# Kernel tuning notes

Measured on AMD Instinct MI355X. Metric: run time of the kernel, lower is better.

## Reference

```python
import jax, jax.numpy as jnp
import numpy as np

K = 32  # knn neighborhood size (hard-coded in get_graph_feature)
EPS_BN = 1e-5


def _bn(x, g, b):
    # batch-norm (training-mode batch stats) over all axes except the last (channel) axis
    axes = tuple(range(x.ndim - 1))
    m = jnp.mean(x, axis=axes, keepdims=True)
    v = jnp.var(x, axis=axes, keepdims=True)
    return (x - m) * jax.lax.rsqrt(v + EPS_BN) * g + b


def _knn_idx(xt, k):
    # xt: [B, N, C] -> indices of k nearest points [B, N, k] (torch topk on -||xi-xj||^2)
    xx = jnp.sum(xt * xt, axis=-1)                       # [B, N]
    inner = jnp.einsum('bnc,bmc->bnm', xt, xt)           # [B, N, N]
    neg_d2 = -(xx[:, :, None] - 2.0 * inner + xx[:, None, :])
    _, idx = jax.lax.top_k(neg_d2, k)
    return idx


def _graph_feature(x, k=K):
    # x: [B, C, N] -> feature [B, N, k, 2C] matching torch cat((neighbors, center))
    xt = jnp.transpose(x, (0, 2, 1))                     # [B, N, C]
    idx = _knn_idx(xt, k)                                # [B, N, k]
    gathered = jax.vmap(lambda a, i: a[i])(xt, idx)      # [B, N, k, C]
    center = jnp.broadcast_to(xt[:, :, None, :], gathered.shape)
    return jnp.concatenate([gathered, center], axis=-1)


def _dgcnn(x, w1, w2, w3, w4, w5, g1, g2, g3, g4, g5, b1, b2, b3, b4, b5):
    # x: [B, 3, N] -> embeddings [B, emb, N]
    feat = _graph_feature(x)                                         # [B, N, K, 6]
    h = jax.nn.relu(_bn(jnp.einsum('bnkc,oc->bnko', feat, w1), g1, b1))
    x1 = jnp.max(h, axis=2)                                          # [B, N, 64]
    h = jax.nn.relu(_bn(jnp.einsum('bnkc,oc->bnko', h, w2), g2, b2))
    x2 = jnp.max(h, axis=2)
    h = jax.nn.relu(_bn(jnp.einsum('bnkc,oc->bnko', h, w3), g3, b3))
    x3 = jnp.max(h, axis=2)
    h = jax.nn.relu(_bn(jnp.einsum('bnkc,oc->bnko', h, w4), g4, b4))
    x4 = jnp.max(h, axis=2)
    cat = jnp.concatenate([x1, x2, x3, x4], axis=-1)                 # [B, N, 512]
    emb = jax.nn.relu(_bn(jnp.einsum('bnc,oc->bno', cat, w5), g5, b5))
    return jnp.transpose(emb, (0, 2, 1))                             # [B, emb, N]


def _pairwise_distance_batch(x, y):
    # x: [B, c, N], y: [B, c, M] -> euclidean distances [B, N, M] (faithful incl. clamp/mask)
    xx = jnp.sum(x * x, axis=1)                          # [B, N]
    yy = jnp.sum(y * y, axis=1)                          # [B, M]
    inner = jnp.einsum('bcn,bcm->bnm', x, y)
    pd = xx[:, :, None] - 2.0 * inner + yy[:, None, :]
    pd_sq = jnp.where(pd > 0.0, pd, 0.0)
    err = (pd_sq <= 0.0).astype(pd.dtype)
    d = jnp.sqrt(pd_sq + err * 1e-16)
    return d * (1.0 - err)


def setup_inputs() -> dict:
    key = jax.random.key(0)
    ks = jax.random.split(key, 20)
    B, N = 4, 2048
    def w(k, o, i):
        return jax.random.normal(k, (o, i), jnp.float32) * (1.0 / np.sqrt(i))
    inp = {
        'src': jax.random.normal(ks[0], (B, 3, N), jnp.float32),
        'tgt': jax.random.normal(ks[1], (B, 3, N), jnp.float32),
        'w1': w(ks[2], 64, 6), 'w2': w(ks[3], 64, 64), 'w3': w(ks[4], 128, 64),
        'w4': w(ks[5], 256, 128), 'w5': w(ks[6], 512, 512),
        'g1': jnp.ones(64), 'g2': jnp.ones(64), 'g3': jnp.ones(128),
        'g4': jnp.ones(256), 'g5': jnp.ones(512),
        'b1': jnp.zeros(64), 'b2': jnp.zeros(64), 'b3': jnp.zeros(128),
        'b4': jnp.zeros(256), 'b5': jnp.zeros(512),
    }
    return inp


def reference(src, tgt, w1, w2, w3, w4, w5, g1, g2, g3, g4, g5, b1, b2, b3, b4, b5):
    params = (w1, w2, w3, w4, w5, g1, g2, g3, g4, g5, b1, b2, b3, b4, b5)
    f_src = _dgcnn(src, *params)                         # [B, emb, N]
    f_tgt = _dgcnn(tgt, *params)                         # [B, emb, N] (siamese)
    d = _pairwise_distance_batch(f_src, f_tgt)           # [B, N, M]
    scores = jax.nn.softmax(-d, axis=-1)                 # soft correspondence
    src_corr = jnp.einsum('bcm,bnm->bcn', tgt, scores)   # tgt @ scores^T, [B, 3, N]
    return src_corr
```

## Files before the change

kernel.cpp:

```cpp
#include <hip/hip_runtime.h>
#include <hip/hip_bf16.h>
#include <math.h>

#define BB 4
#define NN 2048
#define KK 32
#define GG 2
constexpr int BNr = BB * NN;
constexpr int SGr = BB * NN * KK;
constexpr int SR  = GG * SGr;

typedef __hip_bfloat16 bf16;
typedef __attribute__((ext_vector_type(8))) short bf16x8;
typedef __attribute__((ext_vector_type(4))) float f32x4;
__device__ __forceinline__ float b2f(bf16 v) { return __bfloat162float(v); }
__device__ __forceinline__ bf16  f2b(float v) { return __float2bfloat16(v); }
__device__ __forceinline__ short f2bs(float v) { bf16 b = f2b(v); return *(short*)&b; }
__device__ __forceinline__ float bs2f(short s) { bf16 b; *(short*)&b = s; return b2f(b); }

#define SWZ128(b) ((b) ^ ((((b) >> 7) & 7) << 4))
#define SWZ256(b) ((b) ^ ((((b) >> 8) & 7) << 4))

__global__ __launch_bounds__(256) void knn_kernel(const float* __restrict__ src,
                                                  const float* __restrict__ tgt,
                                                  int* __restrict__ idx_out) {
    __shared__ float pts[3 * NN];
    __shared__ float xxs[NN];
    int blk = blockIdx.x;
    int gb = blk >> 9;
    int chunk = blk & 511;
    int g = gb >> 2, b = gb & 3;
    const float* x = (g == 0 ? src : tgt) + (size_t)b * 3 * NN;
    int t = threadIdx.x;
    for (int i = t; i < 3 * NN; i += 256) pts[i] = x[i];
    __syncthreads();
    for (int m = t; m < NN; m += 256) {
        float p0 = pts[m], p1 = pts[NN + m], p2 = pts[2 * NN + m];
        xxs[m] = p0 * p0 + p1 * p1 + p2 * p2;
    }
    __syncthreads();
    int w = t >> 6, l = t & 63;
    int n = chunk * 4 + w;
    float q0 = pts[n], q1 = pts[NN + n], q2 = pts[2 * NN + n];
    float xxn = xxs[n];
    float d2[32];
#pragma unroll
    for (int s = 0; s < 32; ++s) {
        int m = s * 64 + l;
        float dot = q0 * pts[m] + q1 * pts[NN + m] + q2 * pts[2 * NN + m];
        d2[s] = (xxn - 2.0f * dot) + xxs[m];
    }
    float gval[4]; int gslot[4];
#pragma unroll
    for (int G = 0; G < 4; ++G) {
        float v = d2[G * 8]; int sl = G * 8;
#pragma unroll
        for (int s = 1; s < 8; ++s)
            if (d2[G * 8 + s] < v) { v = d2[G * 8 + s]; sl = G * 8 + s; }
        gval[G] = v; gslot[G] = sl;
    }
    int* outp = idx_out + ((size_t)gb * NN + n) * KK;
    for (int k = 0; k < KK; ++k) {
        float bv = fminf(fminf(gval[0], gval[1]), fminf(gval[2], gval[3]));
        float gv = bv;
#pragma unroll
        for (int off = 1; off < 64; off <<= 1) gv = fminf(gv, __shfl_xor(gv, off));
        unsigned long long mask = __ballot(bv == gv);
        int winner = (int)__builtin_ctzll(mask);
        if (l == winner) {
            int grp = (gval[0] == gv) ? 0 : (gval[1] == gv) ? 1 : (gval[2] == gv) ? 2 : 3;
#pragma unroll
            for (int G = 0; G < 4; ++G)
                if (G == grp) {
                    int bs = gslot[G];
                    outp[k] = bs * 64 + l;
#pragma unroll
                    for (int s = 0; s < 8; ++s)
                        if (G * 8 + s == bs) d2[G * 8 + s] = INFINITY;
                    float v = d2[G * 8]; int sl = G * 8;
#pragma unroll
                    for (int s = 1; s < 8; ++s)
                        if (d2[G * 8 + s] < v) { v = d2[G * 8 + s]; sl = G * 8 + s; }
                    gval[G] = v; gslot[G] = sl;
                }
        }
    }
}

__global__ void zero_kernel(float* __restrict__ p, int n) {
    int i = blockIdx.x * 256 + threadIdx.x;
    if (i < n) p[i] = 0.f;
}

__global__ void cvt_all_kernel(const float* __restrict__ w2, const float* __restrict__ w3,
                               const float* __restrict__ w4, const float* __restrict__ w5,
                               bf16* __restrict__ w2b, bf16* __restrict__ w3b,
                               bf16* __restrict__ w4b, bf16* __restrict__ w5b) {
    int i = blockIdx.x * 256 + threadIdx.x;
    if (i < 4096)   w2b[i] = f2b(w2[i]);
    if (i < 8192)   w3b[i] = f2b(w3[i]);
    if (i < 32768)  w4b[i] = f2b(w4[i]);
    if (i < 262144) w5b[i] = f2b(w5[i]);
}

__global__ void finalize_bn_kernel(float* __restrict__ sums, int C,
                                   const float* __restrict__ gamma,
                                   const float* __restrict__ beta,
                                   float cnt, float* __restrict__ params) {
    int i = blockIdx.x * blockDim.x + threadIdx.x;
    if (i >= GG * C) return;
    int g = i / C, c = i - g * C;
    float s  = sums[(g * 512 + c) * 2 + 0];
    float sq = sums[(g * 512 + c) * 2 + 1];
    float mean = s / cnt;
    float var = sq / cnt - mean * mean;
    if (var < 0.f) var = 0.f;
    float sc = gamma[c] * rsqrtf(var + 1e-5f);
    params[(g * 512 + c) * 2 + 0] = sc;
    params[(g * 512 + c) * 2 + 1] = beta[c] - mean * sc;
    sums[(g * 512 + c) * 2 + 0] = 0.f;
    sums[(g * 512 + c) * 2 + 1] = 0.f;
}

template <int MODE>
__global__ __launch_bounds__(256, 3) void l12_mfma(
    const float* __restrict__ src, const float* __restrict__ tgt,
    const float* __restrict__ w1, const bf16* __restrict__ w2b,
    const int* __restrict__ idx, const float* __restrict__ p1,
    bf16* __restrict__ H2, bf16* __restrict__ cat, float* __restrict__ sums) {
    __shared__ char F1s[32768];
    __shared__ char W2s[8192];
    __shared__ float epiA[512];
    __shared__ float epiB[128];
    int tid = threadIdx.x;
    int w = tid >> 6, l = tid & 63, lg = l >> 4, lr = l & 15;
    long long row0 = (long long)blockIdx.x * 256;
    int g = (int)(row0 / SGr);

    epiA[tid] = 0.f; epiA[tid + 256] = 0.f;
    if (MODE == 1) {
        if (tid < 128) epiB[tid] = 0.f;
        for (int s = tid; s < 512; s += 256)
            *(bf16x8*)(W2s + SWZ128(s * 16)) = *(const bf16x8*)(w2b + s * 8);
    }

    bf16x8 af[4];
#pragma unroll
    for (int i = 0; i < 4; ++i) {
        af[i] = (bf16x8){0, 0, 0, 0, 0, 0, 0, 0};
        if (lg == 0) {
            int rr = (int)row0 + w * 64 + 16 * i + lr;
            int nrow = rr >> 5;
            int n = nrow & (NN - 1);
            int gb = nrow >> 11;
            int b = gb & 3, gg = gb >> 2;
            const float* x = (gg ? tgt : src) + (size_t)b * 3 * NN;
            int j = idx[rr];
            af[i][0] = f2bs(x[j]);
            af[i][1] = f2bs(x[NN + j]);
            af[i][2] = f2bs(x[2 * NN + j]);
            af[i][3] = f2bs(x[n]);
            af[i][4] = f2bs(x[NN + n]);
            af[i][5] = f2bs(x[2 * NN + n]);
        }
    }
    bf16x8 bf1[4];
#pragma unroll
    for (int j = 0; j < 4; ++j) {
        bf1[j] = (bf16x8){0, 0, 0, 0, 0, 0, 0, 0};
        if (lg == 0) {
            int o = 16 * j + lr;
#pragma unroll
            for (int c = 0; c < 6; ++c) bf1[j][c] = f2bs(w1[o * 6 + c]);
        }
    }

    f32x4 acc1[4][4] = {};
#pragma unroll
    for (int i = 0; i < 4; ++i)
#pragma unroll
        for (int j = 0; j < 4; ++j)
            acc1[i][j] = __builtin_amdgcn_mfma_f32_16x16x32_bf16(af[i], bf1[j], acc1[i][j], 0, 0, 0);

    __syncthreads();

    if (MODE == 0) {
#pragma unroll
        for (int j = 0; j < 4; ++j) {
            int c = 16 * j + lr;
            float s = 0.f, q = 0.f;
#pragma unroll
            for (int i = 0; i < 4; ++i)
#pragma unroll
                for (int r = 0; r < 4; ++r) { float v = acc1[i][j][r]; s += v; q += v * v; }
            s += __shfl_xor(s, 16); s += __shfl_xor(s, 32);
            q += __shfl_xor(q, 16); q += __shfl_xor(q, 32);
            if (lg == 0) {
                atomicAdd(&epiA[c * 2], s);
                atomicAdd(&epiA[c * 2 + 1], q);
            }
        }
        __syncthreads();
        if (tid < 128) atomicAdd(&sums[g * 1024 + tid], epiA[tid]);
        return;
    }

#pragma unroll
    for (int j = 0; j < 4; ++j) {
        int c = 16 * j + lr;
        float sc = p1[(g * 512 + c) * 2], sh = p1[(g * 512 + c) * 2 + 1];
#pragma unroll
        for (int i = 0; i < 4; ++i) {
            float m = 0.f;
#pragma unroll
            for (int r = 0; r < 4; ++r) {
                float v = fmaf(acc1[i][j][r], sc, sh);
                v = v > 0.f ? v : 0.f;
                m = fmaxf(m, v);
                int rowi = w * 64 + 16 * i + 4 * lg + r;
                *(bf16*)(F1s + SWZ128((rowi * 64 + c) * 2)) = f2b(v);
            }
            int p = 2 * w + (i >> 1);
            atomicMax((int*)epiA + p * 64 + c, __float_as_int(m));
        }
    }
    __syncthreads();

    {
        long long pt0 = row0 >> 5;
        for (int e = tid; e < 512; e += 256) {
            int p = e >> 6, c = e & 63;
            cat[(pt0 + p) * 512 + c] = f2b(__int_as_float(((int*)epiA)[p * 64 + c]));
        }
    }

    f32x4 acc2[4][4] = {};
#pragma unroll
    for (int ks = 0; ks < 2; ++ks) {
        bf16x8 bv[4];
#pragma unroll
        for (int j = 0; j < 4; ++j)
            bv[j] = *(bf16x8*)(W2s + SWZ128(((16 * j + lr) * 64 + ks * 32 + lg * 8) * 2));
#pragma unroll
        for (int i = 0; i < 4; ++i) {
            bf16x8 a = *(bf16x8*)(F1s + SWZ128(((w * 64 + 16 * i + lr) * 64 + ks * 32 + lg * 8) * 2));
#pragma unroll
            for (int j = 0; j < 4; ++j)
                acc2[i][j] = __builtin_amdgcn_mfma_f32_16x16x32_bf16(a, bv[j], acc2[i][j], 0, 0, 0);
        }
    }

#pragma unroll
    for (int j = 0; j < 4; ++j) {
        int c = 16 * j + lr;
        float s = 0.f, q = 0.f;
#pragma unroll
        for (int i = 0; i < 4; ++i)
#pragma unroll
            for (int r = 0; r < 4; ++r) {
                float v = acc2[i][j][r];
                s += v; q += v * v;
                long long gr = row0 + w * 64 + 16 * i + 4 * lg + r;
                H2[gr * 64 + c] = f2b(v);
            }
        s += __shfl_xor(s, 16); s += __shfl_xor(s, 32);
        q += __shfl_xor(q, 16); q += __shfl_xor(q, 32);
        if (lg == 0) {
            atomicAdd(&epiB[c * 2], s);
            atomicAdd(&epiB[c * 2 + 1], q);
        }
    }
    __syncthreads();
    if (tid < 128) atomicAdd(&sums[g * 1024 + tid], epiB[tid]);
}

template <int APPLY>
__global__ __launch_bounds__(512, 2) void chain34_mfma(
    const bf16* __restrict__ H2, const bf16* __restrict__ w3b,
    const bf16* __restrict__ w4b, const float* __restrict__ p2,
    const float* __restrict__ p3, const float* __restrict__ p4,
    bf16* __restrict__ cat, float* __restrict__ sums) {
    extern __shared__ char smem[];
    char* W3s = smem;
    char* W4s = smem + 16384;
    char* A2s = smem + 81920;
    char* F3s = smem + 98304;
    float* P3s = (float*)(smem + 131072);
    float* P4s = (float*)(smem + 132096);
    float* epi = (float*)(smem + 134144);
    float* P2s = (float*)(smem + 138240);

    int tid = threadIdx.x;
    int w = tid >> 6, l = tid & 63, lg = l >> 4, lr = l & 15;
    long long rowB0 = (long long)blockIdx.x * 512;
    int g = (int)(rowB0 / SGr);

    for (int s = tid; s < 1024; s += 512)
        *(bf16x8*)(W3s + SWZ128(s * 16)) = *(const bf16x8*)(w3b + s * 8);
    for (int s = tid; s < 4096; s += 512)
        *(bf16x8*)(W4s + SWZ256(s * 16)) = *(const bf16x8*)(w4b + s * 8);
    if (tid < 256) P3s[tid] = p3[g * 1024 + tid];
    if (tid < 128) P2s[tid] = p2[g * 1024 + tid];
    P4s[tid] = p4 ? p4[g * 1024 + tid] : 0.f;
    if (!APPLY) epi[tid] = 0.f;
    __syncthreads();

    for (int chunk = 0; chunk < 4; ++chunk) {
        long long row0 = rowB0 + chunk * 128;
        for (int s = tid; s < 1024; s += 512) {
            bf16x8 rv = *(const bf16x8*)(H2 + row0 * 64 + s * 8);
            int cb = (s & 7) * 8;
            bf16x8 ov;
#pragma unroll
            for (int e = 0; e < 8; ++e) {
                float v = fmaf(bs2f(rv[e]), P2s[(cb + e) * 2], P2s[(cb + e) * 2 + 1]);
                v = v > 0.f ? v : 0.f;
                ov[e] = f2bs(v);
            }
            *(bf16x8*)(A2s + SWZ128(s * 16)) = ov;
        }
        if (APPLY) { ((int*)epi)[tid] = 0; ((int*)epi)[tid + 512] = 0; }
        __syncthreads();

        f32x4 acc3[8] = {};
#pragma unroll
        for (int ks = 0; ks < 2; ++ks) {
            bf16x8 a = *(bf16x8*)(A2s + SWZ128(((16 * w + lr) * 64 + ks * 32 + lg * 8) * 2));
#pragma unroll
            for (int j = 0; j < 8; ++j) {
                bf16x8 b = *(bf16x8*)(W3s + SWZ128(((16 * j + lr) * 64 + ks * 32 + lg * 8) * 2));
                acc3[j] = __builtin_amdgcn_mfma_f32_16x16x32_bf16(a, b, acc3[j], 0, 0, 0);
            }
        }
#pragma unroll
        for (int j = 0; j < 8; ++j) {
            int c = 16 * j + lr;
            float sc = P3s[c * 2], sh = P3s[c * 2 + 1];
#pragma unroll
            for (int r = 0; r < 4; ++r) {
                float v = fmaf(acc3[j][r], sc, sh);
                v = v > 0.f ? v : 0.f;
                int rowi = 16 * w + 4 * lg + r;
                *(bf16*)(F3s + SWZ256((rowi * 128 + c) * 2)) = f2b(v);
            }
        }
        __syncthreads();

        f32x4 acc4[16] = {};
#pragma unroll
        for (int ks = 0; ks < 4; ++ks) {
            bf16x8 a = *(bf16x8*)(F3s + SWZ256(((16 * w + lr) * 128 + ks * 32 + lg * 8) * 2));
#pragma unroll
            for (int j = 0; j < 16; ++j) {
                bf16x8 b = *(bf16x8*)(W4s + SWZ256(((16 * j + lr) * 128 + ks * 32 + lg * 8) * 2));
                acc4[j] = __builtin_amdgcn_mfma_f32_16x16x32_bf16(a, b, acc4[j], 0, 0, 0);
            }
        }

        if (!APPLY) {
#pragma unroll
            for (int j = 0; j < 16; ++j) {
                int c = 16 * j + lr;
                float s = acc4[j][0] + acc4[j][1] + acc4[j][2] + acc4[j][3];
                float q = acc4[j][0] * acc4[j][0] + acc4[j][1] * acc4[j][1] +
                          acc4[j][2] * acc4[j][2] + acc4[j][3] * acc4[j][3];
                s += __shfl_xor(s, 16); s += __shfl_xor(s, 32);
                q += __shfl_xor(q, 16); q += __shfl_xor(q, 32);
                if (lg == 0) {
                    atomicAdd(&epi[c * 2], s);
                    atomicAdd(&epi[c * 2 + 1], q);
                }
            }
        } else {
#pragma unroll
            for (int j = 0; j < 16; ++j) {
                int c = 16 * j + lr;
                float sc = P4s[c * 2], sh = P4s[c * 2 + 1];
                float m = 0.f;
#pragma unroll
                for (int r = 0; r < 4; ++r) {
                    float v = fmaf(acc4[j][r], sc, sh);
                    v = v > 0.f ? v : 0.f;
                    m = fmaxf(m, v);
                }
                m = fmaxf(m, __shfl_xor(m, 16));
                m = fmaxf(m, __shfl_xor(m, 32));
                if (lg == 0)
                    atomicMax((int*)epi + (w >> 1) * 256 + c, __float_as_int(m));
            }
            __syncthreads();
            long long pt0 = row0 >> 5;
            for (int e = tid; e < 1024; e += 512) {
                int p = e >> 8, c = e & 255;
                cat[(pt0 + p) * 512 + 256 + c] = f2b(__int_as_float(((int*)epi)[p * 256 + c]));
            }
            {
                int p = tid >> 7, c = tid & 127;
                float m = 0.f;
                for (int r = 0; r < 32; ++r)
                    m = fmaxf(m, b2f(*(bf16*)(F3s + SWZ256(((p * 32 + r) * 128 + c) * 2))));
                cat[(pt0 + p) * 512 + 128 + c] = f2b(m);
            }
            __syncthreads();
        }
    }
    if (!APPLY) {
        __syncthreads();
        atomicAdd(&sums[g * 1024 + tid], epi[tid]);
    }
}

template <int MODE, int CH, int BNA>
__global__ __launch_bounds__(256, 4) void mfma_gemm(
    const bf16* __restrict__ A, const bf16* __restrict__ Wt,
    float* __restrict__ OutF, bf16* __restrict__ OutB,
    int Cin, int ldOut, long long sA, long long sW, long long sO,
    int rowsPerGroup, const float* __restrict__ params, float* __restrict__ sums,
    const float* __restrict__ pba, bf16* __restrict__ cat) {
    __shared__ char As[16384];
    __shared__ char Bs[8192];
    __shared__ float epi[128];
    __shared__ float PBs[128];
    __shared__ int x2m[256];
    int tid = threadIdx.x;
    int w = tid >> 6, l = tid & 63, lg = l >> 4, lr = l & 15;
    int bz = blockIdx.z;
    const bf16* Ap = A + (long long)bz * sA;
    const bf16* Wp = Wt + (long long)bz * sW;
    int o0 = blockIdx.y * 64;
    long long rowB0 = (long long)blockIdx.x * (128 * CH);
    int g = (int)(rowB0 / rowsPerGroup);
    if ((MODE == 1 || MODE == 3) && tid < 128) epi[tid] = 0.f;
    if (BNA && tid < 128) PBs[tid] = pba[g * 1024 + tid];
    int wr = (w >> 1) * 64, wc = (w & 1) * 32;

    for (int ch = 0; ch < CH; ++ch) {
        long long row0 = rowB0 + (long long)ch * 128;
        if (BNA) {
            __syncthreads();
            if (tid < 256) x2m[tid] = 0;
        }
        f32x4 acc[4][2] = {};
        for (int k0 = 0; k0 < Cin; k0 += 64) {
            __syncthreads();
            for (int s = tid; s < 1024; s += 256) {
                if (BNA) {
                    bf16x8 rv = *(const bf16x8*)(Ap + (row0 + (s >> 3)) * Cin + k0 + (s & 7) * 8);
                    int cb = k0 + (s & 7) * 8;
                    int pt = (s >> 3) >> 5;
                    bf16x8 ov;
#pragma unroll
                    for (int e = 0; e < 8; ++e) {
                        float v = fmaf(bs2f(rv[e]), PBs[(cb + e) * 2], PBs[(cb + e) * 2 + 1]);
                        v = v > 0.f ? v : 0.f;
                        ov[e] = f2bs(v);
                        atomicMax(&x2m[pt * 64 + cb + e], __float_as_int(v));
                    }
                    *(bf16x8*)(As + SWZ128(s * 16)) = ov;
                } else {
                    *(bf16x8*)(As + SWZ128(s * 16)) =
                        *(const bf16x8*)(Ap + (row0 + (s >> 3)) * Cin + k0 + (s & 7) * 8);
                }
            }
            for (int s = tid; s < 512; s += 256)
                *(bf16x8*)(Bs + SWZ128(s * 16)) =
                    *(const bf16x8*)(Wp + (long long)(o0 + (s >> 3)) * Cin + k0 + (s & 7) * 8);
            __syncthreads();
#pragma unroll
            for (int ks = 0; ks < 2; ++ks) {
                bf16x8 b0 = *(bf16x8*)(Bs + SWZ128(((wc + lr) * 64 + ks * 32 + lg * 8) * 2));
                bf16x8 b1 = *(bf16x8*)(Bs + SWZ128(((wc + 16 + lr) * 64 + ks * 32 + lg * 8) * 2));
#pragma unroll
                for (int i = 0; i < 4; ++i) {
                    bf16x8 a = *(bf16x8*)(As + SWZ128(((wr + 16 * i + lr) * 64 + ks * 32 + lg * 8) * 2));
                    acc[i][0] = __builtin_amdgcn_mfma_f32_16x16x32_bf16(a, b0, acc[i][0], 0, 0, 0);
                    acc[i][1] = __builtin_amdgcn_mfma_f32_16x16x32_bf16(a, b1, acc[i][1], 0, 0, 0);
                }
            }
        }
        if (BNA && blockIdx.y == 0) {
            long long pt0 = row0 >> 5;
            if (tid < 256) {
                int p = tid >> 6, c = tid & 63;
                cat[(pt0 + p) * 512 + 64 + c] = f2b(__int_as_float(x2m[tid]));
            }
        }
        if (MODE == 1 || MODE == 3) {
#pragma unroll
            for (int j = 0; j < 2; ++j) {
                int c = wc + 16 * j + lr;
                float s = 0.f, q = 0.f;
#pragma unroll
                for (int i = 0; i < 4; ++i)
#pragma unroll
                    for (int r = 0; r < 4; ++r) {
                        float v = acc[i][j][r];
                        s += v; q += v * v;
                    }
                s += __shfl_xor(s, 16); s += __shfl_xor(s, 32);
                q += __shfl_xor(q, 16); q += __shfl_xor(q, 32);
                if (lg == 0) {
                    atomicAdd(&epi[c * 2], s);
                    atomicAdd(&epi[c * 2 + 1], q);
                }
            }
        }
        if (MODE == 0 || MODE == 3) {
            float* Op = OutF + (long long)bz * sO;
#pragma unroll
            for (int j = 0; j < 2; ++j) {
                int gc = o0 + wc + 16 * j + lr;
#pragma unroll
                for (int i = 0; i < 4; ++i)
#pragma unroll
                    for (int r = 0; r < 4; ++r) {
                        long long gr = row0 + wr + 16 * i + 4 * lg + r;
                        Op[gr * ldOut + gc] = acc[i][j][r];
                    }
            }
        }
    }
    if (MODE == 1 || MODE == 3) {
        __syncthreads();
        if (tid < 128) atomicAdd(&sums[g * 1024 + o0 * 2 + tid], epi[tid]);
    }
}

__global__ __launch_bounds__(256) void emb_finalize(const float* __restrict__ h5,
                                                    const float* __restrict__ p5,
                                                    bf16* __restrict__ embB,
                                                    float* __restrict__ nrm) {
    __shared__ float red[256];
    int row = blockIdx.x; int t = threadIdx.x;
    int g = row / BNr;
    float s = 0.f;
#pragma unroll
    for (int i = 0; i < 2; ++i) {
        int c = t + i * 256;
        float v = fmaf(h5[(size_t)row * 512 + c], p5[(g * 512 + c) * 2], p5[(g * 512 + c) * 2 + 1]);
        v = v > 0.f ? v : 0.f;
        bf16 bb = f2b(v);
        embB[(size_t)row * 512 + c] = bb;
        float vb = b2f(bb);
        s += vb * vb;
    }
    red[t] = s; __syncthreads();
    for (int st = 128; st > 0; st >>= 1) { if (t < st) red[t] += red[t + st]; __syncthreads(); }
    if (t == 0) nrm[row] = red[0];
}

__global__ __launch_bounds__(256) void corr_kernel(const float* __restrict__ inner,
                                                   const float* __restrict__ nrm,
                                                   const float* __restrict__ tgt,
                                                   float* __restrict__ out) {
    __shared__ float red[256];
    int blk = blockIdx.x;
    int b = blk >> 11, n = blk & (NN - 1);
    int t = threadIdx.x;
    const float* inr = inner + ((size_t)b * NN + n) * NN;
    float xx = nrm[b * NN + n];
    float dloc[8];
    float vmax = -INFINITY;
#pragma unroll
    for (int i = 0; i < 8; ++i) {
        int m = t + i * 256;
        float pd = (xx - 2.f * inr[m]) + nrm[BNr + b * NN + m];
        float d = pd > 0.f ? sqrtf(pd) : 0.f;
        dloc[i] = d;
        vmax = fmaxf(vmax, -d);
    }
    red[t] = vmax; __syncthreads();
    for (int s = 128; s > 0; s >>= 1) { if (t < s) red[t] = fmaxf(red[t], red[t + s]); __syncthreads(); }
    vmax = red[0]; __syncthreads();
    const float* tp = tgt + (size_t)b * 3 * NN;
    float se = 0.f, s0 = 0.f, s1 = 0.f, s2 = 0.f;
#pragma unroll
    for (int i = 0; i < 8; ++i) {
        int m = t + i * 256;
        float p = expf(-dloc[i] - vmax);
        se += p;
        s0 += p * tp[m]; s1 += p * tp[NN + m]; s2 += p * tp[2 * NN + m];
    }
    red[t] = se; __syncthreads();
    for (int s = 128; s > 0; s >>= 1) { if (t < s) red[t] += red[t + s]; __syncthreads(); }
    float tot = red[0]; __syncthreads();
    red[t] = s0; __syncthreads();
    for (int s = 128; s > 0; s >>= 1) { if (t < s) red[t] += red[t + s]; __syncthreads(); }
    float o0v = red[0]; __syncthreads();
    red[t] = s1; __syncthreads();
    for (int s = 128; s > 0; s >>= 1) { if (t < s) red[t] += red[t + s]; __syncthreads(); }
    float o1v = red[0]; __syncthreads();
    red[t] = s2; __syncthreads();
    for (int s = 128; s > 0; s >>= 1) { if (t < s) red[t] += red[t + s]; __syncthreads(); }
    float o2v = red[0];
    if (t == 0) {
        out[(size_t)b * 3 * NN + n]          = o0v / tot;
        out[(size_t)b * 3 * NN + NN + n]     = o1v / tot;
        out[(size_t)b * 3 * NN + 2 * NN + n] = o2v / tot;
    }
}

extern "C" void kernel_launch(void* const* d_in, const int* in_sizes, int n_in,
                              void* d_out, int out_size, void* d_ws, size_t ws_size,
                              hipStream_t stream) {
    const float* src = (const float*)d_in[0];
    const float* tgt = (const float*)d_in[1];
    const float* w1  = (const float*)d_in[2];
    const float* w2  = (const float*)d_in[3];
    const float* w3  = (const float*)d_in[4];
    const float* w4  = (const float*)d_in[5];
    const float* w5  = (const float*)d_in[6];
    const float* g1  = (const float*)d_in[7];
    const float* g2  = (const float*)d_in[8];
    const float* g3  = (const float*)d_in[9];
    const float* g4  = (const float*)d_in[10];
    const float* g5  = (const float*)d_in[11];
    const float* b1  = (const float*)d_in[12];
    const float* b2  = (const float*)d_in[13];
    const float* b3  = (const float*)d_in[14];
    const float* b4  = (const float*)d_in[15];
    const float* b5  = (const float*)d_in[16];
    float* out = (float*)d_out;
    char* ws = (char*)d_ws;
    (void)in_sizes; (void)n_in;

    size_t off = 0;
    auto alloc = [&](size_t bytes) { size_t o = off; off = (off + bytes + 255) & ~(size_t)255; return o; };
    int*   idx  = (int*)(ws + alloc((size_t)SR * 4));
    bf16*  H2   = (bf16*)(ws + alloc((size_t)SR * 64 * 2));
    bf16*  cat  = (bf16*)(ws + alloc((size_t)GG * BNr * 512 * 2));
    bf16*  embB = (bf16*)(ws + alloc((size_t)GG * BNr * 512 * 2));
    float* h5   = (float*)(ws + alloc((size_t)GG * BNr * 512 * 4));
    float* nrm  = (float*)(ws + alloc((size_t)GG * BNr * 4));
    float* sums = (float*)(ws + alloc(2048 * 4));
    float* prm  = (float*)(ws + alloc(5 * 2048 * 4));
    bf16*  w2b  = (bf16*)(ws + alloc(4096 * 2));
    bf16*  w3b  = (bf16*)(ws + alloc(8192 * 2));
    bf16*  w4b  = (bf16*)(ws + alloc(32768 * 2));
    bf16*  w5b  = (bf16*)(ws + alloc(262144 * 2));
    float* P1 = prm, *P2 = prm + 2048, *P3 = prm + 4096, *P4 = prm + 6144, *P5 = prm + 8192;
    float* inner = (float*)H2;

    if (ws_size < off) {
        hipMemsetAsync(d_out, 0, (size_t)out_size * 4, stream);
        return;
    }

    knn_kernel<<<GG * BB * NN / 4, 256, 0, stream>>>(src, tgt, idx);
    cvt_all_kernel<<<1024, 256, 0, stream>>>(w2, w3, w4, w5, w2b, w3b, w4b, w5b);
    zero_kernel<<<8, 256, 0, stream>>>(sums, 2048);

    l12_mfma<0><<<SR / 256, 256, 0, stream>>>(src, tgt, w1, w2b, idx, nullptr, nullptr, nullptr, sums);
    finalize_bn_kernel<<<1, 128, 0, stream>>>(sums, 64, g1, b1, (float)SGr, P1);

    l12_mfma<1><<<SR / 256, 256, 0, stream>>>(src, tgt, w1, w2b, idx, P1, H2, cat, sums);
    finalize_bn_kernel<<<1, 128, 0, stream>>>(sums, 64, g2, b2, (float)SGr, P2);

    mfma_gemm<1, 4, 1><<<dim3(SR / 512, 2, 1), 256, 0, stream>>>(
        H2, w3b, nullptr, nullptr, 64, 0, 0, 0, 0, SGr, nullptr, sums, P2, cat);
    finalize_bn_kernel<<<2, 128, 0, stream>>>(sums, 128, g3, b3, (float)SGr, P3);

    chain34_mfma<0><<<1024, 512, 138752, stream>>>(H2, w3b, w4b, P2, P3, nullptr, nullptr, sums);
    finalize_bn_kernel<<<4, 128, 0, stream>>>(sums, 256, g4, b4, (float)SGr, P4);
    chain34_mfma<1><<<1024, 512, 138752, stream>>>(H2, w3b, w4b, P2, P3, P4, cat, nullptr);

    mfma_gemm<3, 1, 0><<<dim3(GG * BNr / 128, 8, 1), 256, 0, stream>>>(
        cat, w5b, h5, nullptr, 512, 512, 0, 0, 0, BNr, nullptr, sums, nullptr, nullptr);
    finalize_bn_kernel<<<8, 128, 0, stream>>>(sums, 512, g5, b5, (float)BNr, P5);
    emb_finalize<<<GG * BNr, 256, 0, stream>>>(h5, P5, embB, nrm);

    mfma_gemm<0, 1, 0><<<dim3(NN / 128, NN / 64, BB), 256, 0, stream>>>(
        embB, embB + (size_t)BNr * 512, inner, nullptr, 512, 2048,
        (long long)NN * 512, (long long)NN * 512, (long long)NN * NN,
        SGr, nullptr, nullptr, nullptr, nullptr);

    corr_kernel<<<BB * NN, 256, 0, stream>>>(inner, nrm, tgt, out);
}
```

Before: 724.0 us.

## Drop W4 staging from LDS and raise chain34 occupancy with transposed layer-3 MFMA

Layer-4 weights are no longer staged in shared memory; B fragments are read straight from global memory through the caches. This roughly halves LDS use and moves it to static shared arrays, and launch bounds are raised to 4 blocks per CU. The layer-3 MFMA now swaps its operands so each lane holds four consecutive channels, which allows hoisted per-lane BN scale/shift and packed 4-element LDS stores. The cost is repeated global loads of W4 inside the inner loop, plus a tighter register budget from the higher occupancy target that may cause spills given the 64-float accumulator.

```diff
diff --git a/kernel.cpp b/kernel.cpp
--- a/kernel.cpp
+++ b/kernel.cpp
@@ -12,6 +12,7 @@
 
 typedef __hip_bfloat16 bf16;
 typedef __attribute__((ext_vector_type(8))) short bf16x8;
+typedef __attribute__((ext_vector_type(4))) short s16x4;
 typedef __attribute__((ext_vector_type(4))) float f32x4;
 __device__ __forceinline__ float b2f(bf16 v) { return __bfloat162float(v); }
 __device__ __forceinline__ bf16  f2b(float v) { return __float2bfloat16(v); }
@@ -275,20 +276,18 @@
 }
 
 template <int APPLY>
-__global__ __launch_bounds__(512, 2) void chain34_mfma(
+__global__ __launch_bounds__(512, 4) void chain34_mfma(
     const bf16* __restrict__ H2, const bf16* __restrict__ w3b,
     const bf16* __restrict__ w4b, const float* __restrict__ p2,
     const float* __restrict__ p3, const float* __restrict__ p4,
     bf16* __restrict__ cat, float* __restrict__ sums) {
-    extern __shared__ char smem[];
-    char* W3s = smem;
-    char* W4s = smem + 16384;
-    char* A2s = smem + 81920;
-    char* F3s = smem + 98304;
-    float* P3s = (float*)(smem + 131072);
-    float* P4s = (float*)(smem + 132096);
-    float* epi = (float*)(smem + 134144);
-    float* P2s = (float*)(smem + 138240);
+    __shared__ char W3s[16384];
+    __shared__ char A2s[16384];
+    __shared__ char F3s[32768];
+    __shared__ float P2s[128];
+    __shared__ float P3s[256];
+    __shared__ float P4s[512];
+    __shared__ float epi[1024];
 
     int tid = threadIdx.x;
     int w = tid >> 6, l = tid & 63, lg = l >> 4, lr = l & 15;
@@ -297,13 +296,18 @@
 
     for (int s = tid; s < 1024; s += 512)
         *(bf16x8*)(W3s + SWZ128(s * 16)) = *(const bf16x8*)(w3b + s * 8);
-    for (int s = tid; s < 4096; s += 512)
-        *(bf16x8*)(W4s + SWZ256(s * 16)) = *(const bf16x8*)(w4b + s * 8);
     if (tid < 256) P3s[tid] = p3[g * 1024 + tid];
     if (tid < 128) P2s[tid] = p2[g * 1024 + tid];
-    P4s[tid] = p4 ? p4[g * 1024 + tid] : 0.f;
+    P4s[tid & 511] = p4 ? p4[g * 1024 + (tid & 511)] : 0.f;
     if (!APPLY) epi[tid] = 0.f;
     __syncthreads();
+
+    float sc3[4], sh3[4];
+#pragma unroll
+    for (int r = 0; r < 4; ++r) {
+        int c = 16 * w + 4 * lg + r;
+        sc3[r] = P3s[c * 2]; sh3[r] = P3s[c * 2 + 1];
+    }
 
     for (int chunk = 0; chunk < 4; ++chunk) {
         long long row0 = rowB0 + chunk * 128;
@@ -325,24 +329,23 @@
         f32x4 acc3[8] = {};
 #pragma unroll
         for (int ks = 0; ks < 2; ++ks) {
-            bf16x8 a = *(bf16x8*)(A2s + SWZ128(((16 * w + lr) * 64 + ks * 32 + lg * 8) * 2));
+            bf16x8 wf = *(bf16x8*)(W3s + SWZ128(((16 * w + lr) * 64 + ks * 32 + lg * 8) * 2));
 #pragma unroll
             for (int j = 0; j < 8; ++j) {
-                bf16x8 b = *(bf16x8*)(W3s + SWZ128(((16 * j + lr) * 64 + ks * 32 + lg * 8) * 2));
-                acc3[j] = __builtin_amdgcn_mfma_f32_16x16x32_bf16(a, b, acc3[j], 0, 0, 0);
+                bf16x8 a2 = *(bf16x8*)(A2s + SWZ128(((16 * j + lr) * 64 + ks * 32 + lg * 8) * 2));
+                acc3[j] = __builtin_amdgcn_mfma_f32_16x16x32_bf16(wf, a2, acc3[j], 0, 0, 0);
             }
         }
 #pragma unroll
         for (int j = 0; j < 8; ++j) {
-            int c = 16 * j + lr;
-            float sc = P3s[c * 2], sh = P3s[c * 2 + 1];
+            s16x4 pk;
 #pragma unroll
             for (int r = 0; r < 4; ++r) {
-                float v = fmaf(acc3[j][r], sc, sh);
+                float v = fmaf(acc3[j][r], sc3[r], sh3[r]);
                 v = v > 0.f ? v : 0.f;
-                int rowi = 16 * w + 4 * lg + r;
-                *(bf16*)(F3s + SWZ256((rowi * 128 + c) * 2)) = f2b(v);
-            }
+                pk[r] = f2bs(v);
+            }
+            *(s16x4*)(F3s + SWZ256(((16 * j + lr) * 128 + 16 * w + 4 * lg) * 2)) = pk;
         }
         __syncthreads();
 
@@ -352,7 +355,7 @@
             bf16x8 a = *(bf16x8*)(F3s + SWZ256(((16 * w + lr) * 128 + ks * 32 + lg * 8) * 2));
 #pragma unroll
             for (int j = 0; j < 16; ++j) {
-                bf16x8 b = *(bf16x8*)(W4s + SWZ256(((16 * j + lr) * 128 + ks * 32 + lg * 8) * 2));
+                bf16x8 b = *(const bf16x8*)(w4b + (16 * j + lr) * 128 + ks * 32 + lg * 8);
                 acc4[j] = __builtin_amdgcn_mfma_f32_16x16x32_bf16(a, b, acc4[j], 0, 0, 0);
             }
         }
@@ -660,9 +663,9 @@
         H2, w3b, nullptr, nullptr, 64, 0, 0, 0, 0, SGr, nullptr, sums, P2, cat);
     finalize_bn_kernel<<<2, 128, 0, stream>>>(sums, 128, g3, b3, (float)SGr, P3);
 
-    chain34_mfma<0><<<1024, 512, 138752, stream>>>(H2, w3b, w4b, P2, P3, nullptr, nullptr, sums);
+    chain34_mfma<0><<<1024, 512, 0, stream>>>(H2, w3b, w4b, P2, P3, nullptr, nullptr, sums);
     finalize_bn_kernel<<<4, 128, 0, stream>>>(sums, 256, g4, b4, (float)SGr, P4);
-    chain34_mfma<1><<<1024, 512, 138752, stream>>>(H2, w3b, w4b, P2, P3, P4, cat, nullptr);
+    chain34_mfma<1><<<1024, 512, 0, stream>>>(H2, w3b, w4b, P2, P3, P4, cat, nullptr);
 
     mfma_gemm<3, 1, 0><<<dim3(GG * BNr / 128, 8, 1), 256, 0, stream>>>(
         cat, w5b, h5, nullptr, 512, 512, 0, 0, 0, BNr, nullptr, sums, nullptr, nullptr);
```

Result: slower. 1.919 ms (+165.0%).
